# Kernel optimization log

Measured on AMD Instinct MI355X. Metric: run time of the kernel, lower is better.

The kernel has to match this reference:

```python
import jax, jax.numpy as jnp
import numpy as np

NEG_INF = -9e16
SLOPE = 0.2  # leaky relu slope


def setup_inputs() -> dict:
    key = jax.random.key(0)
    k1, k2, k3, k4 = jax.random.split(key, 4)
    N, F_in, H, D = 3072, 512, 8, 64
    h = jax.random.normal(k1, (N, F_in), dtype=jnp.float32)
    adj = jax.random.randint(k2, (N, N), 0, 2, dtype=jnp.int32)
    W = jax.random.normal(k3, (H, F_in, D), dtype=jnp.float32) * (2.0 / (F_in + D)) ** 0.5
    a = jax.random.normal(k4, (H, 2 * D, 1), dtype=jnp.float32) * (2.0 / (2 * D + 1)) ** 0.5
    return {"h": h, "adj": adj, "W": W, "a": a}


def reference(h, adj, W, a):
    # h: [N, F], W: [H, F, D], a: [H, 2D, 1], adj: [N, N]
    H, _, D = W.shape
    ht = jnp.einsum("nf,hfd->hnd", h, W)            # [H, N, D]
    a_src = a[:, :D, 0]                               # [H, D]
    a_dst = a[:, D:, 0]                               # [H, D]
    src = jnp.einsum("hnd,hd->hn", ht, a_src)        # [H, N]
    dst = jnp.einsum("hnd,hd->hn", ht, a_dst)        # [H, N]
    e = src[:, :, None] + dst[:, None, :]             # [H, N, N]
    e = jnp.where(e > 0, e, SLOPE * e)                # leaky relu
    e = jnp.where(adj[None] > 0, e, NEG_INF)
    att = jax.nn.softmax(e, axis=-1)                  # [H, N, N]
    hp = jnp.einsum("hnm,hmd->hnd", att, ht)         # [H, N, D]
    out = jnp.transpose(hp, (1, 0, 2)).reshape(h.shape[0], H * D)  # concat heads
    return (out, att)
```

## Files before the change

kernel.cpp:

```cpp
#include <hip/hip_runtime.h>

#define NN 3072
#define FF 512
#define HH 8
#define DD 64
#define SLOPEV 0.2f
#define CH2 64
#define NC2 (NN/CH2)

typedef __bf16  bf16x8 __attribute__((ext_vector_type(8)));
typedef __bf16  bf16x4 __attribute__((ext_vector_type(4)));
typedef short   s16x8  __attribute__((ext_vector_type(8)));
typedef float   f32x4  __attribute__((ext_vector_type(4)));
typedef unsigned long long u64;

#define MFMA16(a,b,c) __builtin_amdgcn_mfma_f32_16x16x32_bf16((a),(b),(c),0,0,0)

__device__ __forceinline__ short f2bf(float x){ __bf16 b=(__bf16)x; return __builtin_bit_cast(short,b); }
__device__ __forceinline__ float bf2f(short s){ return (float)__builtin_bit_cast(__bf16,s); }
__device__ __forceinline__ bf16x8 ldbf8(const short* p){ return __builtin_bit_cast(bf16x8, *(const s16x8*)p); }

__device__ __forceinline__ void gload16(const void* g, void* l){
  __builtin_amdgcn_global_load_lds(
      (const __attribute__((address_space(1))) void*)(uintptr_t)g,
      (__attribute__((address_space(3))) void*)(uint32_t)(uintptr_t)l, 16, 0, 0);
}

__global__ __launch_bounds__(256) void k_split_h(const float* __restrict__ h,
    short* __restrict__ hhi, short* __restrict__ hlo){
  size_t base = ((size_t)blockIdx.x*256 + threadIdx.x)*8;
  float4 v0 = *(const float4*)(h+base);
  float4 v1 = *(const float4*)(h+base+4);
  float vv[8] = {v0.x,v0.y,v0.z,v0.w,v1.x,v1.y,v1.z,v1.w};
  s16x8 hi, lo;
  #pragma unroll
  for (int j=0;j<8;j++){ short s=f2bf(vv[j]); hi[j]=s; lo[j]=f2bf(vv[j]-bf2f(s)); }
  *(s16x8*)(hhi+base)=hi; *(s16x8*)(hlo+base)=lo;
}

__global__ __launch_bounds__(64) void k_wt(const float* __restrict__ W, const float* __restrict__ a,
    short* __restrict__ wthi, short* __restrict__ wtlo,
    float* __restrict__ wasrc, float* __restrict__ wadst){
  int h = blockIdx.y, f0 = blockIdx.x*8, d = threadIdx.x;
  float asv = a[h*2*DD + d];
  float adv = a[h*2*DD + DD + d];
  s16x8 vh, vl;
  #pragma unroll
  for (int j=0;j<8;j++){
    float v = W[((size_t)h*FF + f0 + j)*DD + d];
    short s = f2bf(v); vh[j]=s; vl[j]=f2bf(v-bf2f(s));
    float ws_ = v*asv, wd_ = v*adv;
    #pragma unroll
    for (int m=1;m<64;m<<=1){ ws_ += __shfl_xor(ws_,m,64); wd_ += __shfl_xor(wd_,m,64); }
    if (d==0){ wasrc[h*FF+f0+j]=ws_; wadst[h*FF+f0+j]=wd_; }
  }
  size_t o = ((size_t)h*DD + d)*FF + f0;
  *(s16x8*)(wthi+o)=vh; *(s16x8*)(wtlo+o)=vl;
}

__global__ __launch_bounds__(256) void k_pack(const int* __restrict__ adj, u64* __restrict__ padj){
  int idx = blockIdx.x*256 + threadIdx.x;
  u64 b = __ballot(adj[idx] > 0);
  if ((threadIdx.x & 63) == 0) padj[idx>>6] = b;
}

__global__ __launch_bounds__(256) void k_srcdst(const float* __restrict__ h,
    const float* __restrict__ wasrc, const float* __restrict__ wadst,
    float* __restrict__ src, float* __restrict__ dst){
  int n = blockIdx.x*4 + (threadIdx.x>>6);
  int lane = threadIdx.x & 63;
  const float* hp = h + (size_t)n*FF + lane*8;
  float4 x0 = *(const float4*)hp, x1 = *(const float4*)(hp+4);
  float xs[8] = {x0.x,x0.y,x0.z,x0.w,x1.x,x1.y,x1.z,x1.w};
  float ps[HH], pd[HH];
  #pragma unroll
  for (int hh=0; hh<HH; hh++){
    const float* sp = wasrc + (size_t)hh*FF + lane*8;
    const float* dp = wadst + (size_t)hh*FF + lane*8;
    float4 s0 = *(const float4*)sp, s1 = *(const float4*)(sp+4);
    float4 t0 = *(const float4*)dp, t1 = *(const float4*)(dp+4);
    ps[hh] = xs[0]*s0.x + xs[1]*s0.y + xs[2]*s0.z + xs[3]*s0.w
           + xs[4]*s1.x + xs[5]*s1.y + xs[6]*s1.z + xs[7]*s1.w;
    pd[hh] = xs[0]*t0.x + xs[1]*t0.y + xs[2]*t0.z + xs[3]*t0.w
           + xs[4]*t1.x + xs[5]*t1.y + xs[6]*t1.z + xs[7]*t1.w;
  }
  #pragma unroll
  for (int m=1;m<64;m<<=1){
    #pragma unroll
    for (int hh=0; hh<HH; hh++){ ps[hh] += __shfl_xor(ps[hh],m,64); pd[hh] += __shfl_xor(pd[hh],m,64); }
  }
  if (lane==0){
    #pragma unroll
    for (int hh=0; hh<HH; hh++){ src[hh*NN+n]=ps[hh]; dst[hh*NN+n]=pd[hh]; }
  }
}

__global__ __launch_bounds__(128) void k_ht(const short* __restrict__ hhi, const short* __restrict__ hlo,
    const short* __restrict__ wthi, const short* __restrict__ wtlo,
    short* __restrict__ hthi, short* __restrict__ htlo){
  int h = blockIdx.y, n0 = blockIdx.x*32;
  int w = threadIdx.x>>6, lane = threadIdx.x&63;
  int r15 = lane&15, g = lane>>4;
  int arow = n0 + w*16 + r15;
  f32x4 acc[4] = {{0.f,0.f,0.f,0.f},{0.f,0.f,0.f,0.f},{0.f,0.f,0.f,0.f},{0.f,0.f,0.f,0.f}};
  const short* ha = hhi + (size_t)arow*FF + g*8;
  const short* la = hlo + (size_t)arow*FF + g*8;
  for (int kk=0; kk<FF; kk+=32){
    bf16x8 ahi = ldbf8(ha+kk), alo = ldbf8(la+kk);
    #pragma unroll
    for (int c=0;c<4;c++){
      size_t bo = ((size_t)h*DD + c*16 + r15)*FF + g*8 + kk;
      bf16x8 bh = ldbf8(wthi + bo), bl = ldbf8(wtlo + bo);
      acc[c] = MFMA16(ahi,bh,acc[c]);
      acc[c] = MFMA16(ahi,bl,acc[c]);
      acc[c] = MFMA16(alo,bh,acc[c]);
    }
  }
  #pragma unroll
  for (int c=0;c<4;c++){
    #pragma unroll
    for (int r=0;r<4;r++){
      float v = acc[c][r];
      short s = f2bf(v); short sl = f2bf(v - bf2f(s));
      int n = n0 + w*16 + g*4 + r;
      size_t o = ((size_t)h*DD + c*16 + r15)*NN + n;
      hthi[o]=s; htlo[o]=sl;
    }
  }
}

__global__ __launch_bounds__(512, 8) void k_att(const u64* __restrict__ padj,
    const float* __restrict__ src, const float* __restrict__ dst,
    const short* __restrict__ hthi, const short* __restrict__ htlo,
    float* __restrict__ dout){
  __shared__ short hA[64][CH2], lA[64][CH2], hB[64][CH2], lB[64][CH2];
  __shared__ short pA[32][CH2], pB[32][CH2];
  const size_t OUTOFF = (size_t)NN*HH*DD;
  int bid = blockIdx.x;
  int h = bid & 7, n0 = (bid >> 3) * 32;
  int t = threadIdx.x;
  int r = t>>4, j = t&15;
  int nrow = n0 + r;
  float srcv = src[h*NN + nrow];
  const float* dsth = dst + h*NN;
  const u64* arow = padj + (size_t)nrow*(NN/64);

  int wv = t>>6, lane = t&63, r15 = lane&15, g = lane>>4;
  int cblk = wv&3, nh = wv>>2;
  int drow = t>>3;
  int sslot = (t&7) ^ (drow&7);
  const short* gh = hthi + ((size_t)(h*DD) + drow)*NN + sslot*8;
  const short* gl = htlo + ((size_t)(h*DD) + drow)*NN + sslot*8;

  gload16(gh, &hA[wv*8][0]);
  gload16(gl, &lA[wv*8][0]);

  float psum = 0.f;
  for (int c=0;c<24;c++){
    u64 w0 = arow[c*2], w1 = arow[c*2+1];
    const float* dp = dsth + c*128 + j*4;
    float4 d0 = *(const float4*)dp, d1 = *(const float4*)(dp+64);
    float dj[8] = {d0.x,d0.y,d0.z,d0.w,d1.x,d1.y,d1.z,d1.w};
    #pragma unroll
    for (int e=0;e<8;e++){
      float ev = srcv + dj[e];
      ev = fmaxf(ev, SLOPEV*ev);
      u64 bits = (e<4) ? w0 : w1;
      float p = ((bits >> (j*4 + (e&3))) & 1ull) ? __expf(ev) : 0.f;
      psum += p;
    }
  }
  #pragma unroll
  for (int m=1;m<16;m<<=1) psum += __shfl_xor(psum, m, 64);
  float inv = (psum > 0.f) ? 1.f/psum : (1.f/(float)NN);
  bool am = !(psum > 0.f);

  f32x4 acc = {0.f,0.f,0.f,0.f};
  float* attrow = dout + OUTOFF + ((size_t)(h*NN + nrow))*NN;
  int aoff0 = (cblk*16 + r15)*(CH2*2);
  int boff0 = (nh*16 + r15)*(CH2*2);
  int csw   = (r15&7)<<4;
  int pofs  = r*(CH2*2) + ((j*8) ^ ((r&7)<<4));

  u64 bits = arow[0];
  const float* dvp = dsth + j*4;
  float4 dv = *(const float4*)dvp;

  #pragma unroll 2
  for (int c=0;c<NC2;c++){
    short (*hc)[CH2]; short (*lc)[CH2]; short (*hn)[CH2]; short (*ln)[CH2]; short (*pc)[CH2];
    if (c&1){ hc=hB; lc=lB; hn=hA; ln=lA; pc=pB; }
    else    { hc=hA; lc=lA; hn=hB; ln=lB; pc=pA; }

    if (c < NC2-1){
      gload16(gh + (c+1)*CH2, &hn[wv*8][0]);
      gload16(gl + (c+1)*CH2, &ln[wv*8][0]);
    }
    u64 bits_n = 0; float4 dv_n = {0,0,0,0};
    if (c < NC2-1){
      bits_n = arow[c+1];
      dv_n = *(const float4*)(dvp + (c+1)*CH2);
    }
    float o[4];
    #pragma unroll
    for (int e=0;e<4;e++){
      float ev = srcv + ((const float*)&dv)[e];
      ev = fmaxf(ev, SLOPEV*ev);
      float p = ((bits >> (j*4 + e)) & 1ull) ? __expf(ev) : 0.f;
      if (am) p = 1.f;
      o[e] = p * inv;
    }
    f32x4 s0 = {o[0],o[1],o[2],o[3]};
    __builtin_nontemporal_store(s0, (f32x4*)(attrow + c*CH2 + j*4));
    bf16x4 pb;
    #pragma unroll
    for (int e=0;e<4;e++) pb[e] = (__bf16)o[e];
    *(bf16x4*)((char*)pc + pofs) = pb;

    __syncthreads();

    const char* hcB = (const char*)hc;
    const char* lcB = (const char*)lc;
    const char* pcB = (const char*)pc;
    #pragma unroll
    for (int ks=0;ks<2;ks++){
      int kb = (g*16 + ks*64) ^ csw;
      bf16x8 bf = *(const bf16x8*)(pcB + boff0 + kb);
      bf16x8 ah = *(const bf16x8*)(hcB + aoff0 + kb);
      bf16x8 al = *(const bf16x8*)(lcB + aoff0 + kb);
      acc = MFMA16(ah, bf, acc);
      acc = MFMA16(al, bf, acc);
    }
    __builtin_amdgcn_s_barrier();

    bits = bits_n; dv = dv_n;
  }

  int n = n0 + nh*16 + r15;
  size_t ob = (size_t)n*(HH*DD) + h*DD + cblk*16 + g*4;
  __builtin_nontemporal_store(acc, (f32x4*)(dout+ob));
}

extern "C" void kernel_launch(void* const* d_in, const int* in_sizes, int n_in,
                              void* d_out, int out_size, void* d_ws, size_t ws_size,
                              hipStream_t stream) {
  const float* h   = (const float*)d_in[0];
  const int*   adj = (const int*)d_in[1];
  const float* W   = (const float*)d_in[2];
  const float* a   = (const float*)d_in[3];
  float* out = (float*)d_out;

  short* hhi  = (short*)d_ws;
  short* hlo  = hhi  + (size_t)NN*FF;
  short* wthi = hlo  + (size_t)NN*FF;
  short* wtlo = wthi + (size_t)HH*DD*FF;
  short* hthi = wtlo + (size_t)HH*DD*FF;
  short* htlo = hthi + (size_t)HH*DD*NN;
  float* wasrc= (float*)(htlo + (size_t)HH*DD*NN);
  float* wadst= wasrc + HH*FF;
  float* srcb = wadst + HH*FF;
  float* dstb = srcb + HH*NN;
  u64*   padj = (u64*)(dstb + HH*NN);

  k_split_h<<<dim3(NN*FF/(256*8)), 256, 0, stream>>>(h, hhi, hlo);
  k_wt     <<<dim3(FF/8, HH), 64, 0, stream>>>(W, a, wthi, wtlo, wasrc, wadst);
  k_pack   <<<dim3(NN*NN/256), 256, 0, stream>>>(adj, padj);
  k_srcdst <<<dim3(NN/4), 256, 0, stream>>>(h, wasrc, wadst, srcb, dstb);
  k_ht     <<<dim3(NN/32, HH), 128, 0, stream>>>(hhi, hlo, wthi, wtlo, hthi, htlo);
  k_att    <<<dim3(NN/32*HH), 512, 0, stream>>>(padj, srcb, dstb, hthi, htlo, out);
}
```

Before: 161.9 us.

## Drop ht low-part split, fuse h split into k_ht, deepen att prefetch

```diff
diff --git a/kernel.cpp b/kernel.cpp
--- a/kernel.cpp
+++ b/kernel.cpp
@@ -26,18 +26,6 @@
       (__attribute__((address_space(3))) void*)(uint32_t)(uintptr_t)l, 16, 0, 0);
 }
 
-__global__ __launch_bounds__(256) void k_split_h(const float* __restrict__ h,
-    short* __restrict__ hhi, short* __restrict__ hlo){
-  size_t base = ((size_t)blockIdx.x*256 + threadIdx.x)*8;
-  float4 v0 = *(const float4*)(h+base);
-  float4 v1 = *(const float4*)(h+base+4);
-  float vv[8] = {v0.x,v0.y,v0.z,v0.w,v1.x,v1.y,v1.z,v1.w};
-  s16x8 hi, lo;
-  #pragma unroll
-  for (int j=0;j<8;j++){ short s=f2bf(vv[j]); hi[j]=s; lo[j]=f2bf(vv[j]-bf2f(s)); }
-  *(s16x8*)(hhi+base)=hi; *(s16x8*)(hlo+base)=lo;
-}
-
 __global__ __launch_bounds__(64) void k_wt(const float* __restrict__ W, const float* __restrict__ a,
     short* __restrict__ wthi, short* __restrict__ wtlo,
     float* __restrict__ wasrc, float* __restrict__ wadst){
@@ -59,9 +47,11 @@
 }
 
 __global__ __launch_bounds__(256) void k_pack(const int* __restrict__ adj, u64* __restrict__ padj){
-  int idx = blockIdx.x*256 + threadIdx.x;
-  u64 b = __ballot(adj[idx] > 0);
-  if ((threadIdx.x & 63) == 0) padj[idx>>6] = b;
+  const int total = NN*NN;
+  for (int idx = blockIdx.x*256 + threadIdx.x; idx < total; idx += gridDim.x*256){
+    u64 b = __ballot(adj[idx] > 0);
+    if ((threadIdx.x & 63) == 0) padj[idx>>6] = b;
+  }
 }
 
 __global__ __launch_bounds__(256) void k_srcdst(const float* __restrict__ h,
@@ -95,21 +85,29 @@
   }
 }
 
-__global__ __launch_bounds__(128) void k_ht(const short* __restrict__ hhi, const short* __restrict__ hlo,
+__global__ __launch_bounds__(128) void k_ht(const float* __restrict__ h,
     const short* __restrict__ wthi, const short* __restrict__ wtlo,
-    short* __restrict__ hthi, short* __restrict__ htlo){
-  int h = blockIdx.y, n0 = blockIdx.x*32;
+    short* __restrict__ hthi){
+  __shared__ short tH[64][40];
+  int hh = blockIdx.y, n0 = blockIdx.x*32;
   int w = threadIdx.x>>6, lane = threadIdx.x&63;
   int r15 = lane&15, g = lane>>4;
   int arow = n0 + w*16 + r15;
   f32x4 acc[4] = {{0.f,0.f,0.f,0.f},{0.f,0.f,0.f,0.f},{0.f,0.f,0.f,0.f},{0.f,0.f,0.f,0.f}};
-  const short* ha = hhi + (size_t)arow*FF + g*8;
-  const short* la = hlo + (size_t)arow*FF + g*8;
+  const float* ha = h + (size_t)arow*FF + g*8;
   for (int kk=0; kk<FF; kk+=32){
-    bf16x8 ahi = ldbf8(ha+kk), alo = ldbf8(la+kk);
+    float4 x0 = *(const float4*)(ha+kk), x1 = *(const float4*)(ha+kk+4);
+    float xv[8] = {x0.x,x0.y,x0.z,x0.w,x1.x,x1.y,x1.z,x1.w};
+    bf16x8 ahi, alo;
+    #pragma unroll
+    for (int e=0;e<8;e++){
+      short s = f2bf(xv[e]);
+      ahi[e] = __builtin_bit_cast(__bf16, s);
+      alo[e] = (__bf16)(xv[e] - bf2f(s));
+    }
     #pragma unroll
     for (int c=0;c<4;c++){
-      size_t bo = ((size_t)h*DD + c*16 + r15)*FF + g*8 + kk;
+      size_t bo = ((size_t)hh*DD + c*16 + r15)*FF + g*8 + kk;
       bf16x8 bh = ldbf8(wthi + bo), bl = ldbf8(wtlo + bo);
       acc[c] = MFMA16(ahi,bh,acc[c]);
       acc[c] = MFMA16(ahi,bl,acc[c]);
@@ -120,20 +118,21 @@
   for (int c=0;c<4;c++){
     #pragma unroll
     for (int r=0;r<4;r++){
-      float v = acc[c][r];
-      short s = f2bf(v); short sl = f2bf(v - bf2f(s));
-      int n = n0 + w*16 + g*4 + r;
-      size_t o = ((size_t)h*DD + c*16 + r15)*NN + n;
-      hthi[o]=s; htlo[o]=sl;
-    }
-  }
+      int dloc = c*16 + r15, nloc = w*16 + g*4 + r;
+      tH[dloc][nloc] = f2bf(acc[c][r]);
+    }
+  }
+  __syncthreads();
+  int row = threadIdx.x>>1, half = threadIdx.x&1;
+  size_t o = ((size_t)hh*DD + row)*NN + n0 + half*16;
+  *(s16x8*)(hthi + o)     = *(const s16x8*)&tH[row][half*16];
+  *(s16x8*)(hthi + o + 8) = *(const s16x8*)&tH[row][half*16+8];
 }
 
 __global__ __launch_bounds__(512, 8) void k_att(const u64* __restrict__ padj,
     const float* __restrict__ src, const float* __restrict__ dst,
-    const short* __restrict__ hthi, const short* __restrict__ htlo,
-    float* __restrict__ dout){
-  __shared__ short hA[64][CH2], lA[64][CH2], hB[64][CH2], lB[64][CH2];
+    const short* __restrict__ hthi, float* __restrict__ dout){
+  __shared__ short hA[64][CH2], hB[64][CH2];
   __shared__ short pA[32][CH2], pB[32][CH2];
   const size_t OUTOFF = (size_t)NN*HH*DD;
   int bid = blockIdx.x;
@@ -150,10 +149,8 @@
   int drow = t>>3;
   int sslot = (t&7) ^ (drow&7);
   const short* gh = hthi + ((size_t)(h*DD) + drow)*NN + sslot*8;
-  const short* gl = htlo + ((size_t)(h*DD) + drow)*NN + sslot*8;
 
   gload16(gh, &hA[wv*8][0]);
-  gload16(gl, &lA[wv*8][0]);
 
   float psum = 0.f;
   for (int c=0;c<24;c++){
@@ -182,25 +179,23 @@
   int csw   = (r15&7)<<4;
   int pofs  = r*(CH2*2) + ((j*8) ^ ((r&7)<<4));
 
-  u64 bits = arow[0];
   const float* dvp = dsth + j*4;
-  float4 dv = *(const float4*)dvp;
+  u64 bits  = arow[0];
+  float4 dv  = *(const float4*)dvp;
+  u64 bits1 = arow[1];
+  float4 dv1 = *(const float4*)(dvp + CH2);
 
   #pragma unroll 2
   for (int c=0;c<NC2;c++){
-    short (*hc)[CH2]; short (*lc)[CH2]; short (*hn)[CH2]; short (*ln)[CH2]; short (*pc)[CH2];
-    if (c&1){ hc=hB; lc=lB; hn=hA; ln=lA; pc=pB; }
-    else    { hc=hA; lc=lA; hn=hB; ln=lB; pc=pA; }
-
-    if (c < NC2-1){
-      gload16(gh + (c+1)*CH2, &hn[wv*8][0]);
-      gload16(gl + (c+1)*CH2, &ln[wv*8][0]);
-    }
-    u64 bits_n = 0; float4 dv_n = {0,0,0,0};
-    if (c < NC2-1){
-      bits_n = arow[c+1];
-      dv_n = *(const float4*)(dvp + (c+1)*CH2);
-    }
+    short (*hc)[CH2] = (c&1)?hB:hA;
+    short (*hn)[CH2] = (c&1)?hA:hB;
+    short (*pc)[CH2] = (c&1)?pB:pA;
+
+    int cs = (c+1 < NC2) ? c+1 : NC2-1;
+    gload16(gh + cs*CH2, &hn[wv*8][0]);
+    int cp = (c+2 < NC2) ? c+2 : NC2-1;
+    u64 bits2 = arow[cp];
+    float4 dv2 = *(const float4*)(dvp + cp*CH2);
     float o[4];
     #pragma unroll
     for (int e=0;e<4;e++){
@@ -217,23 +212,27 @@
     for (int e=0;e<4;e++) pb[e] = (__bf16)o[e];
     *(bf16x4*)((char*)pc + pofs) = pb;
 
-    __syncthreads();
+    __builtin_amdgcn_sched_barrier(0);
+    asm volatile("s_waitcnt vmcnt(7) lgkmcnt(0)" ::: "memory");
+    __builtin_amdgcn_sched_barrier(0);
+    __builtin_amdgcn_s_barrier();
+    __builtin_amdgcn_sched_barrier(0);
 
     const char* hcB = (const char*)hc;
-    const char* lcB = (const char*)lc;
     const char* pcB = (const char*)pc;
     #pragma unroll
     for (int ks=0;ks<2;ks++){
       int kb = (g*16 + ks*64) ^ csw;
       bf16x8 bf = *(const bf16x8*)(pcB + boff0 + kb);
       bf16x8 ah = *(const bf16x8*)(hcB + aoff0 + kb);
-      bf16x8 al = *(const bf16x8*)(lcB + aoff0 + kb);
       acc = MFMA16(ah, bf, acc);
-      acc = MFMA16(al, bf, acc);
-    }
+    }
+    asm volatile("" ::: "memory");
     __builtin_amdgcn_s_barrier();
-
-    bits = bits_n; dv = dv_n;
+    __builtin_amdgcn_sched_barrier(0);
+
+    bits = bits1; bits1 = bits2;
+    dv = dv1; dv1 = dv2;
   }
 
   int n = n0 + nh*16 + r15;
@@ -250,22 +249,18 @@
   const float* a   = (const float*)d_in[3];
   float* out = (float*)d_out;
 
-  short* hhi  = (short*)d_ws;
-  short* hlo  = hhi  + (size_t)NN*FF;
-  short* wthi = hlo  + (size_t)NN*FF;
+  short* wthi = (short*)d_ws;
   short* wtlo = wthi + (size_t)HH*DD*FF;
   short* hthi = wtlo + (size_t)HH*DD*FF;
-  short* htlo = hthi + (size_t)HH*DD*NN;
-  float* wasrc= (float*)(htlo + (size_t)HH*DD*NN);
+  float* wasrc= (float*)(hthi + (size_t)HH*DD*NN);
   float* wadst= wasrc + HH*FF;
   float* srcb = wadst + HH*FF;
   float* dstb = srcb + HH*NN;
   u64*   padj = (u64*)(dstb + HH*NN);
 
-  k_split_h<<<dim3(NN*FF/(256*8)), 256, 0, stream>>>(h, hhi, hlo);
-  k_wt     <<<dim3(FF/8, HH), 64, 0, stream>>>(W, a, wthi, wtlo, wasrc, wadst);
-  k_pack   <<<dim3(NN*NN/256), 256, 0, stream>>>(adj, padj);
-  k_srcdst <<<dim3(NN/4), 256, 0, stream>>>(h, wasrc, wadst, srcb, dstb);
-  k_ht     <<<dim3(NN/32, HH), 128, 0, stream>>>(hhi, hlo, wthi, wtlo, hthi, htlo);
-  k_att    <<<dim3(NN/32*HH), 512, 0, stream>>>(padj, srcb, dstb, hthi, htlo, out);
-}
+  k_wt    <<<dim3(FF/8, HH), 64, 0, stream>>>(W, a, wthi, wtlo, wasrc, wadst);
+  k_pack  <<<dim3(2048), 256, 0, stream>>>(adj, padj);
+  k_srcdst<<<dim3(NN/4), 256, 0, stream>>>(h, wasrc, wadst, srcb, dstb);
+  k_ht    <<<dim3(NN/32, HH), 128, 0, stream>>>(h, wthi, wtlo, hthi);
+  k_att   <<<dim3(NN/32*HH), 512, 0, stream>>>(padj, srcb, dstb, hthi, out);
+}
```

After: 153.5 us. 5.2% less time.
